# Performance work log

Measured on AMD Instinct MI355X. Metric: run time of the kernel, lower is better.

## Reference

```python
import jax, jax.numpy as jnp
import numpy as np

B, S, H = 2, 2048, 1024
NH, HD = 16, 64
SCALE = HD ** -0.5


def setup_inputs() -> dict:
    key = jax.random.key(0)
    k1, k2, k3, k4 = jax.random.split(key, 4)
    hidden_states = jax.random.normal(k1, (B, S, H), dtype=jnp.float32)
    attention_mask = jax.random.randint(k2, (B, S), 0, 2, dtype=jnp.int32)
    # xavier-uniform-ish init scale
    w_qkv = jax.random.normal(k3, (3 * H, H), dtype=jnp.float32) * (2.0 / (H + 3 * H)) ** 0.5
    w_out = jax.random.normal(k4, (H, H), dtype=jnp.float32) * (1.0 / H) ** 0.5
    return {"hidden_states": hidden_states, "attention_mask": attention_mask,
            "w_qkv": w_qkv, "w_out": w_out}


def reference(hidden_states, attention_mask, w_qkv, w_out):
    b, s, _ = hidden_states.shape
    qkv = hidden_states @ w_qkv.T                      # [B,S,3H]
    q, k, v = jnp.split(qkv, 3, axis=-1)
    # [B,S,H] -> [B,NH,S,HD]
    reshape = lambda x: x.reshape(b, s, NH, HD).transpose(0, 2, 1, 3)
    q, k, v = reshape(q), reshape(k), reshape(v)
    scores = jnp.einsum('bhqd,bhkd->bhqk', q, k) * SCALE   # [B,NH,S,S]
    mask = attention_mask[:, None, None, :] == 0           # [B,1,1,S]
    scores = jnp.where(mask, -jnp.inf, scores)
    attn = jax.nn.softmax(scores, axis=-1)                 # dropout p: eval mode -> identity
    out = jnp.einsum('bhqk,bhkd->bhqd', attn, v)           # [B,NH,S,HD]
    out = out.transpose(0, 2, 1, 3).reshape(b, s, H)
    return out @ w_out.T
```

## Files before the change

### kernel.cpp

```cpp
#include <hip/hip_runtime.h>
#include <string.h>


typedef __bf16 bf16x8 __attribute__((ext_vector_type(8)));
typedef float  f32x4  __attribute__((ext_vector_type(4)));

#define NTOK   4096
#define HDIM   1024
#define SEQ    2048
#define NHEAD  16
#define FSHIFT 12.0f

__device__ __forceinline__ float bf2f(unsigned short u) {
    union { unsigned int i; float f; } x;
    x.i = ((unsigned int)u) << 16;
    return x.f;
}
__device__ __forceinline__ unsigned short f2bf(float f) {
    union { __bf16 h; unsigned short u; } x;
    x.h = (__bf16)f;
    return x.u;
}

typedef const __attribute__((address_space(1))) unsigned int* gptr_u32;
typedef __attribute__((address_space(3))) unsigned int* lptr_u32;

__device__ __forceinline__ void async16(const unsigned short* g, unsigned short* l) {
    __builtin_amdgcn_global_load_lds((gptr_u32)g, (lptr_u32)l, 16, 0, 0);
}

__global__ void detect_kernel(const unsigned short* __restrict__ hs, int* __restrict__ flag) {
    __shared__ int bad;
    if (threadIdx.x == 0) bad = 0;
    __syncthreads();
    unsigned int idx = threadIdx.x * 4096u;
    float f = bf2f(hs[idx]);
    if (!(fabsf(f) < 1e4f)) atomicOr(&bad, 1);
    __syncthreads();
    if (threadIdx.x == 0) *flag = bad;
}

__global__ void convert3_kernel(const void* __restrict__ s0, const void* __restrict__ s1,
                                const void* __restrict__ s2, unsigned short* __restrict__ dst,
                                const int* __restrict__ flag) {
    const int isf32 = *flag;
    int g = blockIdx.x * blockDim.x + threadIdx.x;
    const int stride = gridDim.x * blockDim.x;
    for (; g < 1048576; g += stride) {
        int i = g * 8;
        const void* src; int off;
        if (i < 4194304)      { src = s0; off = i; }
        else if (i < 7340032) { src = s1; off = i - 4194304; }
        else                  { src = s2; off = i - 7340032; }
        if (isf32) {
            const float* s = (const float*)src + off;
            unsigned short o[8];
#pragma unroll
            for (int j = 0; j < 8; j++) o[j] = f2bf(s[j]);
            *(uint4*)(dst + i) = *(const uint4*)o;
        } else {
            *(uint4*)(dst + i) = *(const uint4*)((const unsigned short*)src + off);
        }
    }
}

template <int MODE>
__global__ __launch_bounds__(256) void gemm_xwt(
    const unsigned short* __restrict__ X, const unsigned short* __restrict__ W,
    int M, int N, int K,
    unsigned short* __restrict__ q_out, unsigned short* __restrict__ k_out,
    unsigned short* __restrict__ v_out, void* __restrict__ d_out,
    const int* __restrict__ flag) {
    __shared__ __align__(16) unsigned short Xs[128 * 32];
    __shared__ __align__(16) unsigned short Ws[128 * 32];

    const int t = threadIdx.x;
    const int w = t >> 6, lane = t & 63, quad = lane >> 4, lr = lane & 15;
    const int wrow = (w >> 1) * 64, wcol = (w & 1) * 64;
    const int m0 = blockIdx.y * 128, n0 = blockIdx.x * 128;

    f32x4 acc[4][4];
#pragma unroll
    for (int mi = 0; mi < 4; mi++)
#pragma unroll
        for (int ni = 0; ni < 4; ni++) acc[mi][ni] = (f32x4){0.f, 0.f, 0.f, 0.f};

    const int srow = w * 32 + (lane >> 2);
    const int scol = (lane & 3) * 8;
    const unsigned short* xg = X + (size_t)(m0 + srow) * K + scol;
    const unsigned short* wg = W + (size_t)(n0 + srow) * K + scol;
    unsigned short* xl0 = &Xs[w * 1024];
    unsigned short* wl0 = &Ws[w * 1024];

    for (int k0 = 0; k0 < K; k0 += 32) {
        __syncthreads();
        async16(xg + k0, xl0);
        async16(xg + k0 + 16 * K, xl0 + 512);
        async16(wg + k0, wl0);
        async16(wg + k0 + 16 * K, wl0 + 512);
        __syncthreads();
        bf16x8 af[4], bfr[4];
#pragma unroll
        for (int mi = 0; mi < 4; mi++)
            af[mi] = *(bf16x8*)&Xs[(wrow + mi * 16 + lr) * 32 + quad * 8];
#pragma unroll
        for (int ni = 0; ni < 4; ni++)
            bfr[ni] = *(bf16x8*)&Ws[(wcol + ni * 16 + lr) * 32 + quad * 8];
#pragma unroll
        for (int mi = 0; mi < 4; mi++)
#pragma unroll
            for (int ni = 0; ni < 4; ni++)
                acc[mi][ni] = __builtin_amdgcn_mfma_f32_16x16x32_bf16(af[mi], bfr[ni], acc[mi][ni], 0, 0, 0);
    }

    if (MODE == 1) {
        const int isf32 = *flag;
#pragma unroll
        for (int mi = 0; mi < 4; mi++)
#pragma unroll
            for (int ni = 0; ni < 4; ni++)
#pragma unroll
                for (int rr = 0; rr < 4; rr++) {
                    int mrow = m0 + wrow + mi * 16 + quad * 4 + rr;
                    int j = n0 + wcol + ni * 16 + lr;
                    float val = acc[mi][ni][rr];
                    size_t dst = (size_t)mrow * N + j;
                    if (isf32) ((float*)d_out)[dst] = val;
                    else ((unsigned short*)d_out)[dst] = f2bf(val);
                }
    } else {
#pragma unroll
        for (int mi = 0; mi < 4; mi++)
#pragma unroll
            for (int ni = 0; ni < 4; ni++)
#pragma unroll
                for (int rr = 0; rr < 4; rr++) {
                    int mrow = m0 + wrow + mi * 16 + quad * 4 + rr;
                    int j = n0 + wcol + ni * 16 + lr;
                    float val = acc[mi][ni][rr];
                    int which = j >> 10, rem = j & 1023;
                    int nh = rem >> 6, hd = rem & 63;
                    int b = mrow >> 11, s = mrow & 2047;
                    if (which == 0) {
                        size_t dst = ((size_t)(b * NHEAD + nh) * SEQ + s) * 64 + hd;
                        q_out[dst] = f2bf(val * 0.125f);
                    } else if (which == 1) {
                        size_t dst = ((size_t)(b * NHEAD + nh) * SEQ + s) * 64 + hd;
                        k_out[dst] = f2bf(val);
                    } else {
                        size_t dst = ((size_t)(b * NHEAD + nh) * 64 + hd) * SEQ + s;
                        v_out[dst] = f2bf(val);
                    }
                }
    }
}

__global__ __launch_bounds__(256) void flash_attn_mfma(
    const unsigned short* __restrict__ q, const unsigned short* __restrict__ k,
    const unsigned short* __restrict__ vt, const int* __restrict__ mask,
    unsigned short* __restrict__ attn_out) {
    __shared__ __align__(16) unsigned short Ks[64 * 72];
    __shared__ __align__(16) unsigned short Vt[64 * 72];
    __shared__ __align__(16) unsigned short Ps[4 * 16 * 72];
    __shared__ float Msk[64];

    const int t = threadIdx.x;
    const int w = t >> 6, lane = t & 63, quad = lane >> 4, lr = lane & 15;
    const int bh = blockIdx.y, b = bh >> 4, h = bh & 15;
    const int q0 = blockIdx.x * 64;

    const unsigned short* qb = q + (size_t)bh * SEQ * 64;
    const unsigned short* kb = k + (size_t)bh * SEQ * 64;
    const unsigned short* vtb = vt + (size_t)bh * 64 * SEQ;
    const int* mb = mask + b * SEQ;

    const unsigned short* qrow = qb + (size_t)(q0 + w * 16 + lr) * 64 + quad * 8;
    bf16x8 qa0 = *(const bf16x8*)qrow;
    bf16x8 qa1 = *(const bf16x8*)(qrow + 32);

    f32x4 oacc[4];
#pragma unroll
    for (int d = 0; d < 4; d++) oacc[d] = (f32x4){0.f, 0.f, 0.f, 0.f};
    float l_st[4] = {0.f, 0.f, 0.f, 0.f};

    const int sr = t >> 2;
    const int sc = (t & 3) * 16;

    for (int k0 = 0; k0 < SEQ; k0 += 64) {
        const uint4* kp = (const uint4*)(kb + (size_t)(k0 + sr) * 64 + sc);
        const uint4* vp = (const uint4*)(vtb + (size_t)sr * SEQ + k0 + sc);
        uint4 ka = kp[0], kb2 = kp[1];
        uint4 va = vp[0], vb2 = vp[1];
        float mval = 0.f;
        if (t < 64) mval = (mb[k0 + t] == 0) ? -1e30f : 0.f;

        __syncthreads();
        *(uint4*)&Ks[sr * 72 + sc] = ka;
        *(uint4*)&Ks[sr * 72 + sc + 8] = kb2;
        *(uint4*)&Vt[sr * 72 + sc] = va;
        *(uint4*)&Vt[sr * 72 + sc + 8] = vb2;
        if (t < 64) Msk[t] = mval;
        __syncthreads();

        float mcol[4];
#pragma unroll
        for (int nt = 0; nt < 4; nt++) mcol[nt] = Msk[nt * 16 + lr] - FSHIFT;

        f32x4 sacc[4];
#pragma unroll
        for (int nt = 0; nt < 4; nt++) {
            bf16x8 k0f = *(bf16x8*)&Ks[(nt * 16 + lr) * 72 + quad * 8];
            bf16x8 k1f = *(bf16x8*)&Ks[(nt * 16 + lr) * 72 + 32 + quad * 8];
            f32x4 z = (f32x4){0.f, 0.f, 0.f, 0.f};
            z = __builtin_amdgcn_mfma_f32_16x16x32_bf16(qa0, k0f, z, 0, 0, 0);
            sacc[nt] = __builtin_amdgcn_mfma_f32_16x16x32_bf16(qa1, k1f, z, 0, 0, 0);
        }

#pragma unroll
        for (int nt = 0; nt < 4; nt++)
#pragma unroll
            for (int rr = 0; rr < 4; rr++) {
                float p = __expf(sacc[nt][rr] + mcol[nt]);
                l_st[rr] += p;
                Ps[(w * 16 + quad * 4 + rr) * 72 + nt * 16 + lr] = f2bf(p);
            }

        bf16x8 pa0 = *(bf16x8*)&Ps[(w * 16 + lr) * 72 + quad * 8];
        bf16x8 pa1 = *(bf16x8*)&Ps[(w * 16 + lr) * 72 + 32 + quad * 8];
#pragma unroll
        for (int d = 0; d < 4; d++) {
            bf16x8 v0f = *(bf16x8*)&Vt[(d * 16 + lr) * 72 + quad * 8];
            bf16x8 v1f = *(bf16x8*)&Vt[(d * 16 + lr) * 72 + 32 + quad * 8];
            oacc[d] = __builtin_amdgcn_mfma_f32_16x16x32_bf16(pa0, v0f, oacc[d], 0, 0, 0);
            oacc[d] = __builtin_amdgcn_mfma_f32_16x16x32_bf16(pa1, v1f, oacc[d], 0, 0, 0);
        }
    }

    float inv[4];
#pragma unroll
    for (int rr = 0; rr < 4; rr++) {
        float s = l_st[rr];
        s += __shfl_xor(s, 1, 16);
        s += __shfl_xor(s, 2, 16);
        s += __shfl_xor(s, 4, 16);
        s += __shfl_xor(s, 8, 16);
        inv[rr] = 1.0f / s;
    }
#pragma unroll
    for (int d = 0; d < 4; d++)
#pragma unroll
        for (int rr = 0; rr < 4; rr++) {
            size_t tok = (size_t)(b * SEQ + q0 + w * 16 + quad * 4 + rr);
            attn_out[tok * HDIM + h * 64 + d * 16 + lr] = f2bf(oacc[d][rr] * inv[rr]);
        }
}

extern "C" void kernel_launch(void* const* d_in, const int* in_sizes, int n_in,
                              void* d_out, int out_size, void* d_ws, size_t ws_size,
                              hipStream_t stream) {
    const void* hs_raw = d_in[0];
    const int* mask = (const int*)d_in[1];
    const void* wqkv_raw = d_in[2];
    const void* wout_raw = d_in[3];

    char* wsb = (char*)d_ws;
    int* flag = (int*)wsb;
    unsigned short* hs_c = (unsigned short*)(wsb + 256);
    unsigned short* wqkv_c = hs_c + 4194304;
    unsigned short* wout_c = wqkv_c + 3145728;
    unsigned short* qw = wout_c + 1048576;
    unsigned short* kw = qw + 4194304;
    unsigned short* vtw = kw + 4194304;
    unsigned short* ao = vtw + 4194304;

    detect_kernel<<<1, 256, 0, stream>>>((const unsigned short*)hs_raw, flag);
    convert3_kernel<<<1024, 256, 0, stream>>>(hs_raw, wqkv_raw, wout_raw, hs_c, flag);

    gemm_xwt<0><<<dim3(24, 32), 256, 0, stream>>>(hs_c, wqkv_c, NTOK, 3072, 1024,
                                                  qw, kw, vtw, nullptr, flag);
    flash_attn_mfma<<<dim3(32, 32), 256, 0, stream>>>(qw, kw, vtw, mask, ao);
    gemm_xwt<1><<<dim3(8, 32), 256, 0, stream>>>(ao, wout_c, NTOK, 1024, 1024,
                                                 nullptr, nullptr, nullptr, d_out, flag);
}
```

Measured before the change: 225.0 us.

## Keep P in registers via transposed QK^T and fp16 PV MFMA, 128-query tiles

The attention kernel computes S^T (K as the A operand, Q as B) so that each lane's score accumulator maps directly to the B-operand layout of a 16x16x16 fp16 MFMA. P can then feed the PV product straight from registers instead of going through an LDS round trip. V is stored as fp16, Q is prescaled by log2(e)/sqrt(d) so exp2 can replace exp, and each block now handles 128 queries (two 16-row groups per wave) to reuse K/V tiles from LDS. The risks are fp16 range for P and V under the fixed shift with no running max, plus roughly twice the register pressure per wave and half the number of blocks.

```diff
diff --git a/kernel.cpp b/kernel.cpp
--- a/kernel.cpp
+++ b/kernel.cpp
@@ -2,14 +2,16 @@
 #include <string.h>
 
 
-typedef __bf16 bf16x8 __attribute__((ext_vector_type(8)));
-typedef float  f32x4  __attribute__((ext_vector_type(4)));
+typedef __bf16    bf16x8 __attribute__((ext_vector_type(8)));
+typedef _Float16  f16x4  __attribute__((ext_vector_type(4)));
+typedef float     f32x4  __attribute__((ext_vector_type(4)));
 
 #define NTOK   4096
 #define HDIM   1024
 #define SEQ    2048
 #define NHEAD  16
-#define FSHIFT 12.0f
+#define F2SHIFT 4.0f
+#define QSCALE  0.18033688f
 
 __device__ __forceinline__ float bf2f(unsigned short u) {
     union { unsigned int i; float f; } x;
@@ -19,6 +21,11 @@
 __device__ __forceinline__ unsigned short f2bf(float f) {
     union { __bf16 h; unsigned short u; } x;
     x.h = (__bf16)f;
+    return x.u;
+}
+__device__ __forceinline__ unsigned short f2h(float f) {
+    union { _Float16 h; unsigned short u; } x;
+    x.h = (_Float16)f;
     return x.u;
 }
 
@@ -143,56 +150,61 @@
                     int b = mrow >> 11, s = mrow & 2047;
                     if (which == 0) {
                         size_t dst = ((size_t)(b * NHEAD + nh) * SEQ + s) * 64 + hd;
-                        q_out[dst] = f2bf(val * 0.125f);
+                        q_out[dst] = f2bf(val * QSCALE);
                     } else if (which == 1) {
                         size_t dst = ((size_t)(b * NHEAD + nh) * SEQ + s) * 64 + hd;
                         k_out[dst] = f2bf(val);
                     } else {
                         size_t dst = ((size_t)(b * NHEAD + nh) * 64 + hd) * SEQ + s;
-                        v_out[dst] = f2bf(val);
+                        v_out[dst] = f2h(val);
                     }
                 }
     }
 }
 
-__global__ __launch_bounds__(256) void flash_attn_mfma(
+__global__ __launch_bounds__(256) void flash_attn_v3(
     const unsigned short* __restrict__ q, const unsigned short* __restrict__ k,
     const unsigned short* __restrict__ vt, const int* __restrict__ mask,
     unsigned short* __restrict__ attn_out) {
     __shared__ __align__(16) unsigned short Ks[64 * 72];
     __shared__ __align__(16) unsigned short Vt[64 * 72];
-    __shared__ __align__(16) unsigned short Ps[4 * 16 * 72];
-    __shared__ float Msk[64];
+    __shared__ __align__(16) float Msk[80];
 
     const int t = threadIdx.x;
     const int w = t >> 6, lane = t & 63, quad = lane >> 4, lr = lane & 15;
     const int bh = blockIdx.y, b = bh >> 4, h = bh & 15;
-    const int q0 = blockIdx.x * 64;
+    const int q0 = blockIdx.x * 128;
 
     const unsigned short* qb = q + (size_t)bh * SEQ * 64;
     const unsigned short* kb = k + (size_t)bh * SEQ * 64;
     const unsigned short* vtb = vt + (size_t)bh * 64 * SEQ;
     const int* mb = mask + b * SEQ;
 
-    const unsigned short* qrow = qb + (size_t)(q0 + w * 16 + lr) * 64 + quad * 8;
-    bf16x8 qa0 = *(const bf16x8*)qrow;
-    bf16x8 qa1 = *(const bf16x8*)(qrow + 32);
-
-    f32x4 oacc[4];
-#pragma unroll
-    for (int d = 0; d < 4; d++) oacc[d] = (f32x4){0.f, 0.f, 0.f, 0.f};
-    float l_st[4] = {0.f, 0.f, 0.f, 0.f};
+    bf16x8 qf[2][2];
+#pragma unroll
+    for (int qg = 0; qg < 2; qg++) {
+        const unsigned short* qrow = qb + (size_t)(q0 + w * 32 + qg * 16 + lr) * 64 + quad * 8;
+        qf[qg][0] = *(const bf16x8*)qrow;
+        qf[qg][1] = *(const bf16x8*)(qrow + 32);
+    }
+
+    f32x4 oacc[2][4];
+#pragma unroll
+    for (int qg = 0; qg < 2; qg++)
+#pragma unroll
+        for (int dt = 0; dt < 4; dt++) oacc[qg][dt] = (f32x4){0.f, 0.f, 0.f, 0.f};
+    float l_st[2] = {0.f, 0.f};
 
     const int sr = t >> 2;
     const int sc = (t & 3) * 16;
 
-    for (int k0 = 0; k0 < SEQ; k0 += 64) {
-        const uint4* kp = (const uint4*)(kb + (size_t)(k0 + sr) * 64 + sc);
-        const uint4* vp = (const uint4*)(vtb + (size_t)sr * SEQ + k0 + sc);
+    for (int kk0 = 0; kk0 < SEQ; kk0 += 64) {
+        const uint4* kp = (const uint4*)(kb + (size_t)(kk0 + sr) * 64 + sc);
+        const uint4* vp = (const uint4*)(vtb + (size_t)sr * SEQ + kk0 + sc);
         uint4 ka = kp[0], kb2 = kp[1];
         uint4 va = vp[0], vb2 = vp[1];
         float mval = 0.f;
-        if (t < 64) mval = (mb[k0 + t] == 0) ? -1e30f : 0.f;
+        if (t < 64) mval = (mb[kk0 + t] == 0) ? -1e30f : -F2SHIFT;
 
         __syncthreads();
         *(uint4*)&Ks[sr * 72 + sc] = ka;
@@ -202,57 +214,54 @@
         if (t < 64) Msk[t] = mval;
         __syncthreads();
 
-        float mcol[4];
-#pragma unroll
-        for (int nt = 0; nt < 4; nt++) mcol[nt] = Msk[nt * 16 + lr] - FSHIFT;
-
-        f32x4 sacc[4];
-#pragma unroll
-        for (int nt = 0; nt < 4; nt++) {
-            bf16x8 k0f = *(bf16x8*)&Ks[(nt * 16 + lr) * 72 + quad * 8];
-            bf16x8 k1f = *(bf16x8*)&Ks[(nt * 16 + lr) * 72 + 32 + quad * 8];
-            f32x4 z = (f32x4){0.f, 0.f, 0.f, 0.f};
-            z = __builtin_amdgcn_mfma_f32_16x16x32_bf16(qa0, k0f, z, 0, 0, 0);
-            sacc[nt] = __builtin_amdgcn_mfma_f32_16x16x32_bf16(qa1, k1f, z, 0, 0, 0);
+#pragma unroll
+        for (int mt = 0; mt < 4; mt++) {
+            bf16x8 a1h0 = *(bf16x8*)&Ks[(mt * 16 + lr) * 72 + quad * 8];
+            bf16x8 a1h1 = *(bf16x8*)&Ks[(mt * 16 + lr) * 72 + 32 + quad * 8];
+            f16x4 a2[4];
+#pragma unroll
+            for (int dt = 0; dt < 4; dt++)
+                a2[dt] = *(f16x4*)&Vt[(dt * 16 + lr) * 72 + mt * 16 + quad * 4];
+            float4 mv = *(const float4*)&Msk[mt * 16 + quad * 4];
+
+#pragma unroll
+            for (int qg = 0; qg < 2; qg++) {
+                f32x4 z = (f32x4){0.f, 0.f, 0.f, 0.f};
+                z = __builtin_amdgcn_mfma_f32_16x16x32_bf16(a1h0, qf[qg][0], z, 0, 0, 0);
+                z = __builtin_amdgcn_mfma_f32_16x16x32_bf16(a1h1, qf[qg][1], z, 0, 0, 0);
+                f16x4 b2;
+                float p0 = __builtin_amdgcn_exp2f(z[0] + mv.x);
+                float p1 = __builtin_amdgcn_exp2f(z[1] + mv.y);
+                float p2 = __builtin_amdgcn_exp2f(z[2] + mv.z);
+                float p3 = __builtin_amdgcn_exp2f(z[3] + mv.w);
+                l_st[qg] += (p0 + p1) + (p2 + p3);
+                b2[0] = (_Float16)p0; b2[1] = (_Float16)p1;
+                b2[2] = (_Float16)p2; b2[3] = (_Float16)p3;
+#pragma unroll
+                for (int dt = 0; dt < 4; dt++)
+                    oacc[qg][dt] = __builtin_amdgcn_mfma_f32_16x16x16f16(a2[dt], b2, oacc[qg][dt], 0, 0, 0);
+            }
         }
-
-#pragma unroll
-        for (int nt = 0; nt < 4; nt++)
-#pragma unroll
-            for (int rr = 0; rr < 4; rr++) {
-                float p = __expf(sacc[nt][rr] + mcol[nt]);
-                l_st[rr] += p;
-                Ps[(w * 16 + quad * 4 + rr) * 72 + nt * 16 + lr] = f2bf(p);
-            }
-
-        bf16x8 pa0 = *(bf16x8*)&Ps[(w * 16 + lr) * 72 + quad * 8];
-        bf16x8 pa1 = *(bf16x8*)&Ps[(w * 16 + lr) * 72 + 32 + quad * 8];
-#pragma unroll
-        for (int d = 0; d < 4; d++) {
-            bf16x8 v0f = *(bf16x8*)&Vt[(d * 16 + lr) * 72 + quad * 8];
-            bf16x8 v1f = *(bf16x8*)&Vt[(d * 16 + lr) * 72 + 32 + quad * 8];
-            oacc[d] = __builtin_amdgcn_mfma_f32_16x16x32_bf16(pa0, v0f, oacc[d], 0, 0, 0);
-            oacc[d] = __builtin_amdgcn_mfma_f32_16x16x32_bf16(pa1, v1f, oacc[d], 0, 0, 0);
-        }
-    }
-
-    float inv[4];
-#pragma unroll
-    for (int rr = 0; rr < 4; rr++) {
-        float s = l_st[rr];
-        s += __shfl_xor(s, 1, 16);
-        s += __shfl_xor(s, 2, 16);
-        s += __shfl_xor(s, 4, 16);
-        s += __shfl_xor(s, 8, 16);
-        inv[rr] = 1.0f / s;
-    }
-#pragma unroll
-    for (int d = 0; d < 4; d++)
-#pragma unroll
-        for (int rr = 0; rr < 4; rr++) {
-            size_t tok = (size_t)(b * SEQ + q0 + w * 16 + quad * 4 + rr);
-            attn_out[tok * HDIM + h * 64 + d * 16 + lr] = f2bf(oacc[d][rr] * inv[rr]);
-        }
+    }
+
+    float inv[2];
+#pragma unroll
+    for (int qg = 0; qg < 2; qg++) {
+        float s = l_st[qg];
+        s += __shfl_xor(s, 16);
+        s += __shfl_xor(s, 32);
+        inv[qg] = 1.0f / s;
+    }
+#pragma unroll
+    for (int qg = 0; qg < 2; qg++) {
+        size_t tok = (size_t)(b * SEQ + q0 + w * 32 + qg * 16 + lr);
+#pragma unroll
+        for (int dt = 0; dt < 4; dt++)
+#pragma unroll
+            for (int rr = 0; rr < 4; rr++)
+                attn_out[tok * HDIM + h * 64 + dt * 16 + quad * 4 + rr] =
+                    f2bf(oacc[qg][dt][rr] * inv[qg]);
+    }
 }
 
 extern "C" void kernel_launch(void* const* d_in, const int* in_sizes, int n_in,
@@ -278,7 +287,7 @@
 
     gemm_xwt<0><<<dim3(24, 32), 256, 0, stream>>>(hs_c, wqkv_c, NTOK, 3072, 1024,
                                                   qw, kw, vtw, nullptr, flag);
-    flash_attn_mfma<<<dim3(32, 32), 256, 0, stream>>>(qw, kw, vtw, mask, ao);
+    flash_attn_v3<<<dim3(16, 32), 256, 0, stream>>>(qw, kw, vtw, mask, ao);
     gemm_xwt<1><<<dim3(8, 32), 256, 0, stream>>>(ao, wout_c, NTOK, 1024, 1024,
                                                  nullptr, nullptr, nullptr, d_out, flag);
 }
```

Measured after the change: 210.4 us. -6.5%, faster.
